# Performance work log

Hardware: AMD Instinct MI355X
Metric: run time of the kernel (lower is better)

The kernel has to match this reference:

```python
import jax, jax.numpy as jnp
import numpy as np

N_EMBD = 1024
N_HEAD = 16
HEAD_DIM = N_EMBD // N_HEAD
EPS = 1e-5


def setup_inputs() -> dict:
    key = jax.random.key(0)
    ks = jax.random.split(key, 12)
    B, T, E = 4, 2048, N_EMBD
    s = 0.02
    return {
        "x": jax.random.normal(ks[0], (B, T, E), jnp.float32),
        "ln1_g": jnp.ones((E,), jnp.float32),
        "ln1_b": jnp.zeros((E,), jnp.float32),
        "w_attn": jax.random.normal(ks[1], (E, 3 * E), jnp.float32) * s,
        "b_attn": jnp.zeros((3 * E,), jnp.float32),
        "w_attnproj": jax.random.normal(ks[2], (E, E), jnp.float32) * s,
        "b_attnproj": jnp.zeros((E,), jnp.float32),
        "ln2_g": jnp.ones((E,), jnp.float32),
        "ln2_b": jnp.zeros((E,), jnp.float32),
        "w_fc": jax.random.normal(ks[3], (E, 4 * E), jnp.float32) * s,
        "b_fc": jnp.zeros((4 * E,), jnp.float32),
        "w_proj": jax.random.normal(ks[4], (4 * E, E), jnp.float32) * s,
        "b_proj": jnp.zeros((E,), jnp.float32),
    }


def _layernorm(x, g, b):
    mu = jnp.mean(x, axis=-1, keepdims=True)
    var = jnp.mean(jnp.square(x - mu), axis=-1, keepdims=True)
    return (x - mu) * jax.lax.rsqrt(var + EPS) * g + b


def _attention(x, w_attn, b_attn, w_attnproj, b_attnproj):
    B, T, E = x.shape
    qkv = x @ w_attn + b_attn  # [B,T,3E]
    q, k, v = jnp.split(qkv, 3, axis=-1)
    q = q.reshape(B, T, N_HEAD, HEAD_DIM).transpose(0, 2, 1, 3)
    k = k.reshape(B, T, N_HEAD, HEAD_DIM).transpose(0, 2, 1, 3)
    v = v.reshape(B, T, N_HEAD, HEAD_DIM).transpose(0, 2, 1, 3)
    scores = jnp.einsum("bhqd,bhkd->bhqk", q, k) / np.sqrt(HEAD_DIM).astype(np.float32)
    causal = jnp.tril(jnp.ones((T, T), bool))
    scores = jnp.where(causal, scores, -jnp.inf)
    attn = jax.nn.softmax(scores, axis=-1)
    out = jnp.einsum("bhqk,bhkd->bhqd", attn, v)
    out = out.transpose(0, 2, 1, 3).reshape(B, T, E)
    return out @ w_attnproj + b_attnproj


def reference(x, ln1_g, ln1_b, w_attn, b_attn, w_attnproj, b_attnproj,
              ln2_g, ln2_b, w_fc, b_fc, w_proj, b_proj):
    x = x + _attention(_layernorm(x, ln1_g, ln1_b), w_attn, b_attn,
                       w_attnproj, b_attnproj)
    h = _layernorm(x, ln2_g, ln2_b)
    h = jax.nn.gelu(h @ w_fc + b_fc, approximate=False)
    x = x + (h @ w_proj + b_proj)
    return x
```

## Files before the change

kernel.cpp:

```cpp
#include <hip/hip_runtime.h>
#include <math.h>


constexpr int E_    = 1024;
constexpr int NHEAD = 16;
constexpr int BATCH = 4;
constexpr int TSEQ  = 2048;
constexpr int MROWS = BATCH * TSEQ;

typedef unsigned short ushort_t;
typedef short  bf16x8 __attribute__((ext_vector_type(8)));
typedef float  f32x4  __attribute__((ext_vector_type(4)));
typedef unsigned short u16x4 __attribute__((ext_vector_type(4)));
typedef unsigned short u16x8 __attribute__((ext_vector_type(8)));

__device__ __forceinline__ ushort_t f2bf(float f) {
  unsigned u = __float_as_uint(f);
  unsigned r = (u + 0x7fffu + ((u >> 16) & 1u)) >> 16;
  return (ushort_t)r;
}

__device__ __forceinline__ void gload_lds16(const void* g, void* l) {
  __builtin_amdgcn_global_load_lds(
      (const __attribute__((address_space(1))) void*)g,
      (__attribute__((address_space(3))) void*)l, 16, 0, 0);
}

__global__ __launch_bounds__(256) void castT_kernel(const float* __restrict__ W,
                                                    ushort_t* __restrict__ Wt,
                                                    int K, int N) {
  const int n = blockIdx.x * 64 + (threadIdx.x & 63);
  const int k = blockIdx.y * 32 + (threadIdx.x >> 6) * 8;
  ushort_t v[8];
  #pragma unroll
  for (int u = 0; u < 8; ++u) v[u] = f2bf(W[(size_t)(k + u) * N + n]);
  *(u16x8*)&Wt[(size_t)n * K + k] = *(const u16x8*)v;
}

__global__ __launch_bounds__(256) void ln_kernel(const float* __restrict__ x,
                                                 const float* __restrict__ g,
                                                 const float* __restrict__ b,
                                                 ushort_t* __restrict__ y) {
  const int row = blockIdx.x;
  const float4* xr = reinterpret_cast<const float4*>(x + (size_t)row * E_);
  float4 v = xr[threadIdx.x];
  float s  = v.x + v.y + v.z + v.w;
  float ss = v.x * v.x + v.y * v.y + v.z * v.z + v.w * v.w;
  #pragma unroll
  for (int off = 32; off > 0; off >>= 1) {
    s  += __shfl_down(s, off);
    ss += __shfl_down(ss, off);
  }
  __shared__ float red[8];
  __shared__ float stats[2];
  const int wid = threadIdx.x >> 6;
  if ((threadIdx.x & 63) == 0) { red[wid] = s; red[4 + wid] = ss; }
  __syncthreads();
  if (threadIdx.x == 0) {
    float S  = red[0] + red[1] + red[2] + red[3];
    float SS = red[4] + red[5] + red[6] + red[7];
    float mu  = S * (1.0f / E_);
    float var = SS * (1.0f / E_) - mu * mu;
    stats[0] = mu;
    stats[1] = rsqrtf(var + 1e-5f);
  }
  __syncthreads();
  const float mu = stats[0], rstd = stats[1];
  float4 gv = reinterpret_cast<const float4*>(g)[threadIdx.x];
  float4 bv = reinterpret_cast<const float4*>(b)[threadIdx.x];
  u16x4 o;
  o[0] = f2bf((v.x - mu) * rstd * gv.x + bv.x);
  o[1] = f2bf((v.y - mu) * rstd * gv.y + bv.y);
  o[2] = f2bf((v.z - mu) * rstd * gv.z + bv.z);
  o[3] = f2bf((v.w - mu) * rstd * gv.w + bv.w);
  *(u16x4*)(y + (size_t)row * E_ + threadIdx.x * 4) = o;
}

template <int GELU, int RES, int OBF>
__global__ __launch_bounds__(256) void gemm_kernel(
    const ushort_t* __restrict__ A, const ushort_t* __restrict__ Wt,
    const float* __restrict__ bias, const float* __restrict__ res,
    void* __restrict__ Cout, int M, int N, int K) {
  constexpr int BK = 64;
  __shared__ ushort_t As[128][BK];
  __shared__ ushort_t Bs[128][BK];

  const int t    = threadIdx.x;
  const int lane = t & 63;
  const int wave = t >> 6;
  const int wr   = wave >> 1, wc = wave & 1;
  const int bm   = blockIdx.y * 128, bn = blockIdx.x * 128;

  const f32x4 zero = {0.f, 0.f, 0.f, 0.f};
  f32x4 acc[4][4];
  #pragma unroll
  for (int mi = 0; mi < 4; ++mi)
    #pragma unroll
    for (int ni = 0; ni < 4; ++ni) acc[mi][ni] = zero;

  const int srow  = 32 * wave + (lane >> 3);
  const int skoff = (lane & 7) * 8;
  const ushort_t* gA = A  + (size_t)(bm + srow) * K + skoff;
  const ushort_t* gB = Wt + (size_t)(bn + srow) * K + skoff;

  for (int k0 = 0; k0 < K; k0 += BK) {
    #pragma unroll
    for (int i = 0; i < 4; ++i) {
      gload_lds16(gA + (size_t)(i * 8) * K + k0, &As[32 * wave + i * 8][0]);
      gload_lds16(gB + (size_t)(i * 8) * K + k0, &Bs[32 * wave + i * 8][0]);
    }
    __syncthreads();

    #pragma unroll
    for (int kk = 0; kk < 2; ++kk) {
      bf16x8 af[4], bfr[4];
      #pragma unroll
      for (int mi = 0; mi < 4; ++mi)
        af[mi] = *(const bf16x8*)&As[wr * 64 + mi * 16 + (lane & 15)]
                                    [kk * 32 + (lane >> 4) * 8];
      #pragma unroll
      for (int ni = 0; ni < 4; ++ni)
        bfr[ni] = *(const bf16x8*)&Bs[wc * 64 + ni * 16 + (lane & 15)]
                                     [kk * 32 + (lane >> 4) * 8];
      #pragma unroll
      for (int mi = 0; mi < 4; ++mi)
        #pragma unroll
        for (int ni = 0; ni < 4; ++ni)
          acc[mi][ni] = __builtin_amdgcn_mfma_f32_16x16x32_bf16(
              af[mi], bfr[ni], acc[mi][ni], 0, 0, 0);
    }
    __syncthreads();
  }

  float biasv[4];
  #pragma unroll
  for (int ni = 0; ni < 4; ++ni)
    biasv[ni] = bias[bn + wc * 64 + ni * 16 + (lane & 15)];
  const int ccol = bn + wc * 64 + (lane & 15);

  #pragma unroll
  for (int mi = 0; mi < 4; ++mi) {
    #pragma unroll
    for (int j = 0; j < 4; ++j) {
      const int row = bm + wr * 64 + mi * 16 + (lane >> 4) * 4 + j;
      const size_t rbase = (size_t)row * N;
      #pragma unroll
      for (int ni = 0; ni < 4; ++ni) {
        float v = acc[mi][ni][j] + biasv[ni];
        if (GELU) v = 0.5f * v * (1.0f + erff(v * 0.70710678118654752f));
        if (RES)  v += res[rbase + ccol + ni * 16];
        if (OBF)  ((ushort_t*)Cout)[rbase + ccol + ni * 16] = f2bf(v);
        else      ((float*)Cout)[rbase + ccol + ni * 16] = v;
      }
    }
  }
}

__global__ __launch_bounds__(256) void attn_kernel(const ushort_t* __restrict__ qkv,
                                                   ushort_t* __restrict__ out) {
  __shared__ ushort_t Ks[2][64 * 64];
  __shared__ ushort_t Vt[64 * 64];
  __shared__ ushort_t Ps[4][32 * 64];

  const int qb  = (int)gridDim.x - 1 - (int)blockIdx.x;
  const int b   = blockIdx.y >> 4;
  const int hd  = blockIdx.y & 15;
  const int t   = threadIdx.x;
  const int lane = t & 63, w = t >> 6;
  const int l15 = lane & 15, l4 = lane >> 4;

  const size_t rs3 = 3 * E_;
  const ushort_t* base = qkv + (size_t)b * TSEQ * rs3 + hd * 64;
  const int q0w = qb * 128 + w * 32;

  const int srow = t >> 2;
  const int sc0  = (t & 3) * 16;

  bf16x8 qf[2][2];
  #pragma unroll
  for (int qs = 0; qs < 2; ++qs)
    #pragma unroll
    for (int kk = 0; kk < 2; ++kk)
      qf[qs][kk] = *(const bf16x8*)(base +
          (size_t)(q0w + qs * 16 + l15) * rs3 + kk * 32 + l4 * 8);

  float mrun[2], lrun[2];
  f32x4 oacc[2][4];
  #pragma unroll
  for (int qs = 0; qs < 2; ++qs) {
    mrun[qs] = -INFINITY; lrun[qs] = 0.f;
    #pragma unroll
    for (int c = 0; c < 4; ++c) oacc[qs][c] = f32x4{0.f, 0.f, 0.f, 0.f};
  }

  u16x8 v0, v1;

  auto stageK = [&](int kt, int buf) {
    #pragma unroll
    for (int c = 0; c < 2; ++c) {
      const int lrow  = w * 16 + c * 8 + (lane >> 3);
      const int chunk = (lane & 7) ^ (lane >> 3);
      gload_lds16(base + E_ + (size_t)(kt * 64 + lrow) * rs3 + chunk * 8,
                  &Ks[buf][(w * 16 + c * 8) * 64]);
    }
  };
  auto loadV = [&](int kt) {
    const ushort_t* vsrc = base + 2 * E_ + (size_t)(kt * 64 + srow) * rs3 + sc0;
    v0 = *(const u16x8*)vsrc;
    v1 = *(const u16x8*)(vsrc + 8);
  };
  auto writeVt = [&]() {
    #pragma unroll
    for (int j = 0; j < 8; ++j) {
      const int d0 = sc0 + j;
      const int d1 = sc0 + 8 + j;
      Vt[d0 * 64 + (srow ^ (((d0 + (d0 >> 4)) & 7) << 3))] = v0[j];
      Vt[d1 * 64 + (srow ^ (((d1 + (d1 >> 4)) & 7) << 3))] = v1[j];
    }
  };

  stageK(0, 0);
  loadV(0);
  writeVt();
  __syncthreads();

  const int nt = 2 * qb + 2;
  int cur = 0;
  const f32x4 zero = {0.f, 0.f, 0.f, 0.f};

  for (int kt = 0; kt < nt; ++kt) {
    if (kt + 1 < nt) { stageK(kt + 1, cur ^ 1); loadV(kt + 1); }

    f32x4 s[2][4];
    #pragma unroll
    for (int ct = 0; ct < 4; ++ct) {
      const int krow = ct * 16 + l15;
      const int ksw  = (krow & 7) << 3;
      bf16x8 kf0 = *(const bf16x8*)&Ks[cur][krow * 64 + ((l4 * 8) ^ ksw)];
      bf16x8 kf1 = *(const bf16x8*)&Ks[cur][krow * 64 + ((32 + l4 * 8) ^ ksw)];
      #pragma unroll
      for (int qs = 0; qs < 2; ++qs) {
        f32x4 acc = __builtin_amdgcn_mfma_f32_16x16x32_bf16(kf0, qf[qs][0], zero, 0, 0, 0);
        s[qs][ct] = __builtin_amdgcn_mfma_f32_16x16x32_bf16(kf1, qf[qs][1], acc, 0, 0, 0);
      }
    }

    const int ktb = kt * 64;
    const bool domask = (ktb + 63 > q0w);
    #pragma unroll
    for (int qs = 0; qs < 2; ++qs)
      #pragma unroll
      for (int ct = 0; ct < 4; ++ct) {
        s[qs][ct] *= 0.125f;
        if (domask) {
          const int q = q0w + qs * 16 + l15;
          #pragma unroll
          for (int r = 0; r < 4; ++r)
            if (ktb + ct * 16 + l4 * 4 + r > q) s[qs][ct][r] = -INFINITY;
        }
      }

    float escq[2];
    #pragma unroll
    for (int qs = 0; qs < 2; ++qs) {
      float mt = s[qs][0][0];
      #pragma unroll
      for (int ct = 0; ct < 4; ++ct)
        #pragma unroll
        for (int r = 0; r < 4; ++r) mt = fmaxf(mt, s[qs][ct][r]);
      mt = fmaxf(mt, __shfl_xor(mt, 16));
      mt = fmaxf(mt, __shfl_xor(mt, 32));
      const float mnew = fmaxf(mrun[qs], mt);
      escq[qs] = __expf(mrun[qs] - mnew);
      float rs = 0.f;
      #pragma unroll
      for (int ct = 0; ct < 4; ++ct)
        #pragma unroll
        for (int r = 0; r < 4; ++r) {
          const float pv = __expf(s[qs][ct][r] - mnew);
          s[qs][ct][r] = pv;
          rs += pv;
        }
      rs += __shfl_xor(rs, 16);
      rs += __shfl_xor(rs, 32);
      lrun[qs] = lrun[qs] * escq[qs] + rs;
      mrun[qs] = mnew;
    }

    #pragma unroll
    for (int qs = 0; qs < 2; ++qs)
      #pragma unroll
      for (int r = 0; r < 4; ++r) {
        const float eo = __shfl(escq[qs], l4 * 4 + r);
        #pragma unroll
        for (int ct2 = 0; ct2 < 4; ++ct2) oacc[qs][ct2][r] *= eo;
      }

    const int psw = (l15 & 7) << 3;
    #pragma unroll
    for (int qs = 0; qs < 2; ++qs)
      #pragma unroll
      for (int ct = 0; ct < 4; ++ct) {
        u16x4 pk;
        #pragma unroll
        for (int r = 0; r < 4; ++r) pk[r] = f2bf(s[qs][ct][r]);
        *(u16x4*)&Ps[w][(qs * 16 + l15) * 64 + ((ct * 16 + l4 * 4) ^ psw)] = pk;
      }

    bf16x8 pa[2][2];
    #pragma unroll
    for (int qs = 0; qs < 2; ++qs)
      #pragma unroll
      for (int kk = 0; kk < 2; ++kk)
        pa[qs][kk] = *(const bf16x8*)&Ps[w][(qs * 16 + l15) * 64 +
                                            ((kk * 32 + l4 * 8) ^ psw)];
    #pragma unroll
    for (int ct2 = 0; ct2 < 4; ++ct2) {
      const int d   = ct2 * 16 + l15;
      const int vsw = ((d + (d >> 4)) & 7) << 3;
      bf16x8 vb0 = *(const bf16x8*)&Vt[d * 64 + ((l4 * 8) ^ vsw)];
      bf16x8 vb1 = *(const bf16x8*)&Vt[d * 64 + ((32 + l4 * 8) ^ vsw)];
      #pragma unroll
      for (int qs = 0; qs < 2; ++qs) {
        oacc[qs][ct2] = __builtin_amdgcn_mfma_f32_16x16x32_bf16(
            pa[qs][0], vb0, oacc[qs][ct2], 0, 0, 0);
        oacc[qs][ct2] = __builtin_amdgcn_mfma_f32_16x16x32_bf16(
            pa[qs][1], vb1, oacc[qs][ct2], 0, 0, 0);
      }
    }

    __syncthreads();
    if (kt + 1 < nt) writeVt();
    __syncthreads();
    cur ^= 1;
  }

  #pragma unroll
  for (int qs = 0; qs < 2; ++qs)
    #pragma unroll
    for (int r = 0; r < 4; ++r) {
      const float lr  = __shfl(lrun[qs], l4 * 4 + r);
      const float inv = 1.0f / lr;
      const int qg = q0w + qs * 16 + l4 * 4 + r;
      ushort_t* dst = out + (size_t)(b * TSEQ + qg) * E_ + hd * 64 + l15;
      #pragma unroll
      for (int ct2 = 0; ct2 < 4; ++ct2)
        dst[ct2 * 16] = f2bf(oacc[qs][ct2][r] * inv);
    }
}

extern "C" void kernel_launch(void* const* d_in, const int* in_sizes, int n_in,
                              void* d_out, int out_size, void* d_ws, size_t ws_size,
                              hipStream_t stream) {
  const float* x          = (const float*)d_in[0];
  const float* ln1_g      = (const float*)d_in[1];
  const float* ln1_b      = (const float*)d_in[2];
  const float* w_attn     = (const float*)d_in[3];
  const float* b_attn     = (const float*)d_in[4];
  const float* w_attnproj = (const float*)d_in[5];
  const float* b_attnproj = (const float*)d_in[6];
  const float* ln2_g      = (const float*)d_in[7];
  const float* ln2_b      = (const float*)d_in[8];
  const float* w_fc       = (const float*)d_in[9];
  const float* b_fc       = (const float*)d_in[10];
  const float* w_proj     = (const float*)d_in[11];
  const float* b_proj     = (const float*)d_in[12];
  float* out = (float*)d_out;

  char* ws = (char*)d_ws;
  const size_t MB = 1024 * 1024;
  ushort_t* qkv      = (ushort_t*)ws;
  ushort_t* h_bf     = (ushort_t*)ws;
  ushort_t* xn       = (ushort_t*)(ws + 64 * MB);
  ushort_t* attnout  = (ushort_t*)(ws + 80 * MB);
  float*    x1       = (float*)(ws + 96 * MB);
  ushort_t* w_attnT  = (ushort_t*)(ws + 128 * MB);
  ushort_t* w_aprojT = w_attnT  + (size_t)3 * E_ * E_;
  ushort_t* w_fcT    = w_aprojT + (size_t)E_ * E_;
  ushort_t* w_projT  = w_fcT    + (size_t)4 * E_ * E_;

  castT_kernel<<<dim3(3 * E_ / 64, E_ / 32), 256, 0, stream>>>(w_attn, w_attnT, E_, 3 * E_);
  castT_kernel<<<dim3(E_ / 64, E_ / 32), 256, 0, stream>>>(w_attnproj, w_aprojT, E_, E_);
  castT_kernel<<<dim3(4 * E_ / 64, E_ / 32), 256, 0, stream>>>(w_fc, w_fcT, E_, 4 * E_);
  castT_kernel<<<dim3(E_ / 64, 4 * E_ / 32), 256, 0, stream>>>(w_proj, w_projT, 4 * E_, E_);

  ln_kernel<<<MROWS, 256, 0, stream>>>(x, ln1_g, ln1_b, xn);
  gemm_kernel<0, 0, 1><<<dim3(3 * E_ / 128, MROWS / 128), 256, 0, stream>>>(
      xn, w_attnT, b_attn, nullptr, qkv, MROWS, 3 * E_, E_);
  attn_kernel<<<dim3(TSEQ / 128, BATCH * NHEAD), 256, 0, stream>>>(qkv, attnout);
  gemm_kernel<0, 1, 0><<<dim3(E_ / 128, MROWS / 128), 256, 0, stream>>>(
      attnout, w_aprojT, b_attnproj, x, x1, MROWS, E_, E_);
  ln_kernel<<<MROWS, 256, 0, stream>>>(x1, ln2_g, ln2_b, xn);
  gemm_kernel<1, 0, 1><<<dim3(4 * E_ / 128, MROWS / 128), 256, 0, stream>>>(
      xn, w_fcT, b_fc, nullptr, h_bf, MROWS, 4 * E_, E_);
  gemm_kernel<0, 1, 0><<<dim3(E_ / 128, MROWS / 128), 256, 0, stream>>>(
      h_bf, w_projT, b_proj, x1, out, MROWS, E_, 4 * E_);
}
```

Baseline: 659.2 us.

## Use larger double-buffered GEMM tiles and lazy-rescale exp2 flash attention

Replaces the 128x128 single-buffered GEMM with a templated 256xBN, 512-thread kernel that double-buffers LDS tiles through dynamic shared memory, so the next K tile loads while the current one is computed. The attention kernel double-buffers V^T to drop one barrier per iteration and skips fully masked tiles per wave. It also folds log2(e) into the score scale so exp2f can be used, and rescales the running max only when it grows past a threshold. The larger tiles cut the GEMM grids, especially the N=1024 projections, which may hurt occupancy and wave balance on the many-CU device. The lazy rescale bounds unnormalized values rather than keeping them at most 1 before the bf16 cast.

```diff
diff --git a/kernel.cpp b/kernel.cpp
--- a/kernel.cpp
+++ b/kernel.cpp
@@ -76,76 +76,86 @@
   *(u16x4*)(y + (size_t)row * E_ + threadIdx.x * 4) = o;
 }
 
-template <int GELU, int RES, int OBF>
-__global__ __launch_bounds__(256) void gemm_kernel(
+template <int BN, int WM, int WN, int GELU, int RES, int OBF>
+__global__ __launch_bounds__(512) void gemm2_kernel(
     const ushort_t* __restrict__ A, const ushort_t* __restrict__ Wt,
     const float* __restrict__ bias, const float* __restrict__ res,
     void* __restrict__ Cout, int M, int N, int K) {
-  constexpr int BK = 64;
-  __shared__ ushort_t As[128][BK];
-  __shared__ ushort_t Bs[128][BK];
-
-  const int t    = threadIdx.x;
-  const int lane = t & 63;
-  const int wave = t >> 6;
-  const int wr   = wave >> 1, wc = wave & 1;
-  const int bm   = blockIdx.y * 128, bn = blockIdx.x * 128;
-
-  const f32x4 zero = {0.f, 0.f, 0.f, 0.f};
-  f32x4 acc[4][4];
-  #pragma unroll
-  for (int mi = 0; mi < 4; ++mi)
-    #pragma unroll
-    for (int ni = 0; ni < 4; ++ni) acc[mi][ni] = zero;
-
-  const int srow  = 32 * wave + (lane >> 3);
-  const int skoff = (lane & 7) * 8;
-  const ushort_t* gA = A  + (size_t)(bm + srow) * K + skoff;
-  const ushort_t* gB = Wt + (size_t)(bn + srow) * K + skoff;
-
+  constexpr int BM = 256, BK = 64;
+  constexpr int WMR = BM / WM;
+  constexpr int WNC = BN / WN;
+  constexpr int MR  = WMR / 16;
+  constexpr int NR  = WNC / 16;
+  extern __shared__ ushort_t smem[];
+  ushort_t* As = smem;
+  ushort_t* Bs = smem + 2 * BM * BK;
+
+  const int t = threadIdx.x, lane = t & 63, w = t >> 6;
+  const int wr = w / WN, wc = w % WN;
+  const int bm = blockIdx.y * BM, bn = blockIdx.x * BN;
+  const int l15 = lane & 15, l4 = lane >> 4;
+
+  f32x4 acc[MR][NR];
+  #pragma unroll
+  for (int mi = 0; mi < MR; ++mi)
+    #pragma unroll
+    for (int ni = 0; ni < NR; ++ni) acc[mi][ni] = f32x4{0.f, 0.f, 0.f, 0.f};
+
+  const ushort_t* gA = A  + (size_t)(bm + (t >> 3)) * K + (t & 7) * 8;
+  const ushort_t* gB = Wt + (size_t)(bn + (t >> 3)) * K + (t & 7) * 8;
+
+  auto stage = [&](int buf, int k0) {
+    #pragma unroll
+    for (int i = 0; i < BM / 64; ++i)
+      gload_lds16(gA + (size_t)(i * 64) * K + k0,
+                  As + buf * BM * BK + (i * 64 + w * 8) * BK);
+    #pragma unroll
+    for (int i = 0; i < BN / 64; ++i)
+      gload_lds16(gB + (size_t)(i * 64) * K + k0,
+                  Bs + buf * BN * BK + (i * 64 + w * 8) * BK);
+  };
+
+  stage(0, 0);
+  __syncthreads();
+  int cur = 0;
   for (int k0 = 0; k0 < K; k0 += BK) {
-    #pragma unroll
-    for (int i = 0; i < 4; ++i) {
-      gload_lds16(gA + (size_t)(i * 8) * K + k0, &As[32 * wave + i * 8][0]);
-      gload_lds16(gB + (size_t)(i * 8) * K + k0, &Bs[32 * wave + i * 8][0]);
+    if (k0 + BK < K) stage(cur ^ 1, k0 + BK);
+    #pragma unroll
+    for (int kk = 0; kk < 2; ++kk) {
+      bf16x8 af[MR], bv[NR];
+      #pragma unroll
+      for (int mi = 0; mi < MR; ++mi)
+        af[mi] = *(const bf16x8*)&As[cur * BM * BK +
+                 (wr * WMR + mi * 16 + l15) * BK + kk * 32 + l4 * 8];
+      #pragma unroll
+      for (int ni = 0; ni < NR; ++ni)
+        bv[ni] = *(const bf16x8*)&Bs[cur * BN * BK +
+                 (wc * WNC + ni * 16 + l15) * BK + kk * 32 + l4 * 8];
+      #pragma unroll
+      for (int mi = 0; mi < MR; ++mi)
+        #pragma unroll
+        for (int ni = 0; ni < NR; ++ni)
+          acc[mi][ni] = __builtin_amdgcn_mfma_f32_16x16x32_bf16(
+              af[mi], bv[ni], acc[mi][ni], 0, 0, 0);
     }
     __syncthreads();
-
-    #pragma unroll
-    for (int kk = 0; kk < 2; ++kk) {
-      bf16x8 af[4], bfr[4];
-      #pragma unroll
-      for (int mi = 0; mi < 4; ++mi)
-        af[mi] = *(const bf16x8*)&As[wr * 64 + mi * 16 + (lane & 15)]
-                                    [kk * 32 + (lane >> 4) * 8];
-      #pragma unroll
-      for (int ni = 0; ni < 4; ++ni)
-        bfr[ni] = *(const bf16x8*)&Bs[wc * 64 + ni * 16 + (lane & 15)]
-                                     [kk * 32 + (lane >> 4) * 8];
-      #pragma unroll
-      for (int mi = 0; mi < 4; ++mi)
-        #pragma unroll
-        for (int ni = 0; ni < 4; ++ni)
-          acc[mi][ni] = __builtin_amdgcn_mfma_f32_16x16x32_bf16(
-              af[mi], bfr[ni], acc[mi][ni], 0, 0, 0);
-    }
-    __syncthreads();
-  }
-
-  float biasv[4];
-  #pragma unroll
-  for (int ni = 0; ni < 4; ++ni)
-    biasv[ni] = bias[bn + wc * 64 + ni * 16 + (lane & 15)];
-  const int ccol = bn + wc * 64 + (lane & 15);
-
-  #pragma unroll
-  for (int mi = 0; mi < 4; ++mi) {
+    cur ^= 1;
+  }
+
+  float biasv[NR];
+  #pragma unroll
+  for (int ni = 0; ni < NR; ++ni)
+    biasv[ni] = bias[bn + wc * WNC + ni * 16 + l15];
+  const int ccol = bn + wc * WNC + l15;
+
+  #pragma unroll
+  for (int mi = 0; mi < MR; ++mi) {
     #pragma unroll
     for (int j = 0; j < 4; ++j) {
-      const int row = bm + wr * 64 + mi * 16 + (lane >> 4) * 4 + j;
+      const int row = bm + wr * WMR + mi * 16 + l4 * 4 + j;
       const size_t rbase = (size_t)row * N;
       #pragma unroll
-      for (int ni = 0; ni < 4; ++ni) {
+      for (int ni = 0; ni < NR; ++ni) {
         float v = acc[mi][ni][j] + biasv[ni];
         if (GELU) v = 0.5f * v * (1.0f + erff(v * 0.70710678118654752f));
         if (RES)  v += res[rbase + ccol + ni * 16];
@@ -159,8 +169,11 @@
 __global__ __launch_bounds__(256) void attn_kernel(const ushort_t* __restrict__ qkv,
                                                    ushort_t* __restrict__ out) {
   __shared__ ushort_t Ks[2][64 * 64];
-  __shared__ ushort_t Vt[64 * 64];
+  __shared__ ushort_t Vt[2][64 * 64];
   __shared__ ushort_t Ps[4][32 * 64];
+
+  constexpr float CSCL = 0.18033688011112042f;
+  constexpr float THR2 = 11.5415603f;
 
   const int qb  = (int)gridDim.x - 1 - (int)blockIdx.x;
   const int b   = blockIdx.y >> 4;
@@ -174,7 +187,7 @@
   const int q0w = qb * 128 + w * 32;
 
   const int srow = t >> 2;
-  const int sc0  = (t & 3) * 16;
+  const int sc0  = (t & 3) << 4;
 
   bf16x8 qf[2][2];
   #pragma unroll
@@ -195,6 +208,11 @@
 
   u16x8 v0, v1;
 
+  auto loadV = [&](int kt) {
+    const ushort_t* vsrc = base + 2 * E_ + (size_t)(kt * 64 + srow) * rs3 + sc0;
+    v0 = *(const u16x8*)vsrc;
+    v1 = *(const u16x8*)(vsrc + 8);
+  };
   auto stageK = [&](int kt, int buf) {
     #pragma unroll
     for (int c = 0; c < 2; ++c) {
@@ -204,24 +222,19 @@
                   &Ks[buf][(w * 16 + c * 8) * 64]);
     }
   };
-  auto loadV = [&](int kt) {
-    const ushort_t* vsrc = base + 2 * E_ + (size_t)(kt * 64 + srow) * rs3 + sc0;
-    v0 = *(const u16x8*)vsrc;
-    v1 = *(const u16x8*)(vsrc + 8);
-  };
-  auto writeVt = [&]() {
+  auto writeVt = [&](int buf) {
     #pragma unroll
     for (int j = 0; j < 8; ++j) {
       const int d0 = sc0 + j;
       const int d1 = sc0 + 8 + j;
-      Vt[d0 * 64 + (srow ^ (((d0 + (d0 >> 4)) & 7) << 3))] = v0[j];
-      Vt[d1 * 64 + (srow ^ (((d1 + (d1 >> 4)) & 7) << 3))] = v1[j];
+      Vt[buf][d0 * 64 + (srow ^ (((d0 + (d0 >> 4)) & 7) << 3))] = v0[j];
+      Vt[buf][d1 * 64 + (srow ^ (((d1 + (d1 >> 4)) & 7) << 3))] = v1[j];
     }
   };
 
+  loadV(0);
   stageK(0, 0);
-  loadV(0);
-  writeVt();
+  writeVt(0);
   __syncthreads();
 
   const int nt = 2 * qb + 2;
@@ -229,108 +242,109 @@
   const f32x4 zero = {0.f, 0.f, 0.f, 0.f};
 
   for (int kt = 0; kt < nt; ++kt) {
-    if (kt + 1 < nt) { stageK(kt + 1, cur ^ 1); loadV(kt + 1); }
-
-    f32x4 s[2][4];
-    #pragma unroll
-    for (int ct = 0; ct < 4; ++ct) {
-      const int krow = ct * 16 + l15;
-      const int ksw  = (krow & 7) << 3;
-      bf16x8 kf0 = *(const bf16x8*)&Ks[cur][krow * 64 + ((l4 * 8) ^ ksw)];
-      bf16x8 kf1 = *(const bf16x8*)&Ks[cur][krow * 64 + ((32 + l4 * 8) ^ ksw)];
-      #pragma unroll
-      for (int qs = 0; qs < 2; ++qs) {
-        f32x4 acc = __builtin_amdgcn_mfma_f32_16x16x32_bf16(kf0, qf[qs][0], zero, 0, 0, 0);
-        s[qs][ct] = __builtin_amdgcn_mfma_f32_16x16x32_bf16(kf1, qf[qs][1], acc, 0, 0, 0);
-      }
-    }
+    if (kt + 1 < nt) { loadV(kt + 1); stageK(kt + 1, cur ^ 1); }
 
     const int ktb = kt * 64;
-    const bool domask = (ktb + 63 > q0w);
-    #pragma unroll
-    for (int qs = 0; qs < 2; ++qs)
+    if (ktb <= q0w + 31) {
+      f32x4 s[2][4];
       #pragma unroll
       for (int ct = 0; ct < 4; ++ct) {
-        s[qs][ct] *= 0.125f;
-        if (domask) {
-          const int q = q0w + qs * 16 + l15;
-          #pragma unroll
-          for (int r = 0; r < 4; ++r)
-            if (ktb + ct * 16 + l4 * 4 + r > q) s[qs][ct][r] = -INFINITY;
+        const int krow = ct * 16 + l15;
+        const int ksw  = (krow & 7) << 3;
+        bf16x8 kf0 = *(const bf16x8*)&Ks[cur][krow * 64 + ((l4 * 8) ^ ksw)];
+        bf16x8 kf1 = *(const bf16x8*)&Ks[cur][krow * 64 + ((32 + l4 * 8) ^ ksw)];
+        #pragma unroll
+        for (int qs = 0; qs < 2; ++qs) {
+          f32x4 a0 = __builtin_amdgcn_mfma_f32_16x16x32_bf16(kf0, qf[qs][0], zero, 0, 0, 0);
+          s[qs][ct] = __builtin_amdgcn_mfma_f32_16x16x32_bf16(kf1, qf[qs][1], a0, 0, 0, 0);
         }
       }
 
-    float escq[2];
-    #pragma unroll
-    for (int qs = 0; qs < 2; ++qs) {
-      float mt = s[qs][0][0];
-      #pragma unroll
-      for (int ct = 0; ct < 4; ++ct)
-        #pragma unroll
-        for (int r = 0; r < 4; ++r) mt = fmaxf(mt, s[qs][ct][r]);
-      mt = fmaxf(mt, __shfl_xor(mt, 16));
-      mt = fmaxf(mt, __shfl_xor(mt, 32));
-      const float mnew = fmaxf(mrun[qs], mt);
-      escq[qs] = __expf(mrun[qs] - mnew);
-      float rs = 0.f;
-      #pragma unroll
-      for (int ct = 0; ct < 4; ++ct)
-        #pragma unroll
-        for (int r = 0; r < 4; ++r) {
-          const float pv = __expf(s[qs][ct][r] - mnew);
-          s[qs][ct][r] = pv;
-          rs += pv;
+      const bool domask = (ktb + 63 > q0w);
+      #pragma unroll
+      for (int qs = 0; qs < 2; ++qs)
+        #pragma unroll
+        for (int ct = 0; ct < 4; ++ct) {
+          s[qs][ct] *= CSCL;
+          if (domask) {
+            const int q = q0w + qs * 16 + l15;
+            #pragma unroll
+            for (int r = 0; r < 4; ++r)
+              if (ktb + ct * 16 + l4 * 4 + r > q) s[qs][ct][r] = -INFINITY;
+          }
         }
-      rs += __shfl_xor(rs, 16);
-      rs += __shfl_xor(rs, 32);
-      lrun[qs] = lrun[qs] * escq[qs] + rs;
-      mrun[qs] = mnew;
-    }
-
-    #pragma unroll
-    for (int qs = 0; qs < 2; ++qs)
-      #pragma unroll
-      for (int r = 0; r < 4; ++r) {
-        const float eo = __shfl(escq[qs], l4 * 4 + r);
-        #pragma unroll
-        for (int ct2 = 0; ct2 < 4; ++ct2) oacc[qs][ct2][r] *= eo;
+
+      #pragma unroll
+      for (int qs = 0; qs < 2; ++qs) {
+        float pmax = s[qs][0][0];
+        #pragma unroll
+        for (int ct = 0; ct < 4; ++ct)
+          #pragma unroll
+          for (int r = 0; r < 4; ++r) pmax = fmaxf(pmax, s[qs][ct][r]);
+        pmax = fmaxf(pmax, __shfl_xor(pmax, 16));
+        pmax = fmaxf(pmax, __shfl_xor(pmax, 32));
+        if (!__all(pmax - mrun[qs] <= THR2)) {
+          const float mnew = fmaxf(mrun[qs], pmax);
+          const float esc  = exp2f(mrun[qs] - mnew);
+          mrun[qs] = mnew;
+          lrun[qs] *= esc;
+          #pragma unroll
+          for (int r = 0; r < 4; ++r) {
+            const float eo = __shfl(esc, l4 * 4 + r);
+            #pragma unroll
+            for (int c = 0; c < 4; ++c) oacc[qs][c][r] *= eo;
+          }
+        }
+        float rs = 0.f;
+        #pragma unroll
+        for (int ct = 0; ct < 4; ++ct)
+          #pragma unroll
+          for (int r = 0; r < 4; ++r) {
+            const float pv = exp2f(s[qs][ct][r] - mrun[qs]);
+            s[qs][ct][r] = pv;
+            rs += pv;
+          }
+        rs += __shfl_xor(rs, 16);
+        rs += __shfl_xor(rs, 32);
+        lrun[qs] += rs;
       }
 
-    const int psw = (l15 & 7) << 3;
-    #pragma unroll
-    for (int qs = 0; qs < 2; ++qs)
-      #pragma unroll
-      for (int ct = 0; ct < 4; ++ct) {
-        u16x4 pk;
-        #pragma unroll
-        for (int r = 0; r < 4; ++r) pk[r] = f2bf(s[qs][ct][r]);
-        *(u16x4*)&Ps[w][(qs * 16 + l15) * 64 + ((ct * 16 + l4 * 4) ^ psw)] = pk;
+      const int psw = (l15 & 7) << 3;
+      #pragma unroll
+      for (int qs = 0; qs < 2; ++qs)
+        #pragma unroll
+        for (int ct = 0; ct < 4; ++ct) {
+          u16x4 pk;
+          #pragma unroll
+          for (int r = 0; r < 4; ++r) pk[r] = f2bf(s[qs][ct][r]);
+          *(u16x4*)&Ps[w][(qs * 16 + l15) * 64 + ((ct * 16 + l4 * 4) ^ psw)] = pk;
+        }
+
+      bf16x8 pa[2][2];
+      #pragma unroll
+      for (int qs = 0; qs < 2; ++qs)
+        #pragma unroll
+        for (int kk = 0; kk < 2; ++kk)
+          pa[qs][kk] = *(const bf16x8*)&Ps[w][(qs * 16 + l15) * 64 +
+                                              ((kk * 32 + l4 * 8) ^ psw)];
+
+      #pragma unroll
+      for (int ct2 = 0; ct2 < 4; ++ct2) {
+        const int d   = ct2 * 16 + l15;
+        const int vsw = ((d + (d >> 4)) & 7) << 3;
+        bf16x8 vb0 = *(const bf16x8*)&Vt[cur][d * 64 + ((l4 * 8) ^ vsw)];
+        bf16x8 vb1 = *(const bf16x8*)&Vt[cur][d * 64 + ((32 + l4 * 8) ^ vsw)];
+        #pragma unroll
+        for (int qs = 0; qs < 2; ++qs) {
+          oacc[qs][ct2] = __builtin_amdgcn_mfma_f32_16x16x32_bf16(
+              pa[qs][0], vb0, oacc[qs][ct2], 0, 0, 0);
+          oacc[qs][ct2] = __builtin_amdgcn_mfma_f32_16x16x32_bf16(
+              pa[qs][1], vb1, oacc[qs][ct2], 0, 0, 0);
+        }
       }
-
-    bf16x8 pa[2][2];
-    #pragma unroll
-    for (int qs = 0; qs < 2; ++qs)
-      #pragma unroll
-      for (int kk = 0; kk < 2; ++kk)
-        pa[qs][kk] = *(const bf16x8*)&Ps[w][(qs * 16 + l15) * 64 +
-                                            ((kk * 32 + l4 * 8) ^ psw)];
-    #pragma unroll
-    for (int ct2 = 0; ct2 < 4; ++ct2) {
-      const int d   = ct2 * 16 + l15;
-      const int vsw = ((d + (d >> 4)) & 7) << 3;
-      bf16x8 vb0 = *(const bf16x8*)&Vt[d * 64 + ((l4 * 8) ^ vsw)];
-      bf16x8 vb1 = *(const bf16x8*)&Vt[d * 64 + ((32 + l4 * 8) ^ vsw)];
-      #pragma unroll
-      for (int qs = 0; qs < 2; ++qs) {
-        oacc[qs][ct2] = __builtin_amdgcn_mfma_f32_16x16x32_bf16(
-            pa[qs][0], vb0, oacc[qs][ct2], 0, 0, 0);
-        oacc[qs][ct2] = __builtin_amdgcn_mfma_f32_16x16x32_bf16(
-            pa[qs][1], vb1, oacc[qs][ct2], 0, 0, 0);
-      }
-    }
-
-    __syncthreads();
-    if (kt + 1 < nt) writeVt();
+    }
+
+    if (kt + 1 < nt) writeVt(cur ^ 1);
     __syncthreads();
     cur ^= 1;
   }
@@ -379,20 +393,29 @@
   ushort_t* w_fcT    = w_aprojT + (size_t)E_ * E_;
   ushort_t* w_projT  = w_fcT    + (size_t)4 * E_ * E_;
 
+  constexpr int SM256 = (256 + 256) * 64 * 2 * 2;
+  constexpr int SM128 = (256 + 128) * 64 * 2 * 2;
+  hipFuncSetAttribute((const void*)gemm2_kernel<256, 2, 4, 0, 0, 1>,
+                      hipFuncAttributeMaxDynamicSharedMemorySize, SM256);
+  hipFuncSetAttribute((const void*)gemm2_kernel<256, 2, 4, 1, 0, 1>,
+                      hipFuncAttributeMaxDynamicSharedMemorySize, SM256);
+  hipFuncSetAttribute((const void*)gemm2_kernel<128, 4, 2, 0, 1, 0>,
+                      hipFuncAttributeMaxDynamicSharedMemorySize, SM128);
+
   castT_kernel<<<dim3(3 * E_ / 64, E_ / 32), 256, 0, stream>>>(w_attn, w_attnT, E_, 3 * E_);
   castT_kernel<<<dim3(E_ / 64, E_ / 32), 256, 0, stream>>>(w_attnproj, w_aprojT, E_, E_);
   castT_kernel<<<dim3(4 * E_ / 64, E_ / 32), 256, 0, stream>>>(w_fc, w_fcT, E_, 4 * E_);
   castT_kernel<<<dim3(E_ / 64, 4 * E_ / 32), 256, 0, stream>>>(w_proj, w_projT, 4 * E_, E_);
 
   ln_kernel<<<MROWS, 256, 0, stream>>>(x, ln1_g, ln1_b, xn);
-  gemm_kernel<0, 0, 1><<<dim3(3 * E_ / 128, MROWS / 128), 256, 0, stream>>>(
+  gemm2_kernel<256, 2, 4, 0, 0, 1><<<dim3(3 * E_ / 256, MROWS / 256), 512, SM256, stream>>>(
       xn, w_attnT, b_attn, nullptr, qkv, MROWS, 3 * E_, E_);
   attn_kernel<<<dim3(TSEQ / 128, BATCH * NHEAD), 256, 0, stream>>>(qkv, attnout);
-  gemm_kernel<0, 1, 0><<<dim3(E_ / 128, MROWS / 128), 256, 0, stream>>>(
+  gemm2_kernel<128, 4, 2, 0, 1, 0><<<dim3(E_ / 128, MROWS / 256), 512, SM128, stream>>>(
       attnout, w_aprojT, b_attnproj, x, x1, MROWS, E_, E_);
   ln_kernel<<<MROWS, 256, 0, stream>>>(x1, ln2_g, ln2_b, xn);
-  gemm_kernel<1, 0, 1><<<dim3(4 * E_ / 128, MROWS / 128), 256, 0, stream>>>(
+  gemm2_kernel<256, 2, 4, 1, 0, 1><<<dim3(4 * E_ / 256, MROWS / 256), 512, SM256, stream>>>(
       xn, w_fcT, b_fc, nullptr, h_bf, MROWS, 4 * E_, E_);
-  gemm_kernel<0, 1, 0><<<dim3(E_ / 128, MROWS / 128), 256, 0, stream>>>(
+  gemm2_kernel<128, 4, 2, 0, 1, 0><<<dim3(E_ / 128, MROWS / 256), 512, SM128, stream>>>(
       h_bf, w_projT, b_proj, x1, out, MROWS, E_, 4 * E_);
 }
```

Result: faster. 641.7 us (-2.6%).
